# Kernel optimization log

Measured on AMD Instinct MI355X. Metric: run time of the kernel, lower is better.

## Reference

```python
import jax, jax.numpy as jnp
import numpy as np

B, T, C, H, TT = 8, 1024, 512, 8, 4  # batch, seq, n_embd, n_head, total_timestep
D = C // H


def setup_inputs() -> dict:
    key = jax.random.key(0)
    ks = jax.random.split(key, 4)
    s = 1.0 / np.sqrt(C)
    return {
        "x": jax.random.normal(ks[0], (B, T, C), jnp.float32),
        "padding_mask": jax.random.bernoulli(ks[1], 0.1, (TT, T)),  # bool
        "W_qkv": jax.random.normal(ks[2], (C, 3 * C), jnp.float32) * s,
        "b_qkv": jnp.zeros((3 * C,), jnp.float32),
        "W_proj": jax.random.normal(ks[3], (C, C), jnp.float32) * s,
        "b_proj": jnp.zeros((C,), jnp.float32),
    }


def reference(x, padding_mask, W_qkv, b_qkv, W_proj, b_proj):
    # fused QKV projection
    qkv = x @ W_qkv + b_qkv                       # [B,T,3C]
    q, k, v = jnp.split(qkv, 3, axis=-1)
    q = q.reshape(B, T, H, D)
    k = k.reshape(B, T, H, D)
    v = v.reshape(B, T, H, D)

    # mask: causal OR padding (True = attend), replicating torch semantics
    causal = jnp.tril(jnp.ones((T, T), bool))                 # [T,T]
    m = causal[None] | padding_mask[:, :, None]               # [TT,T,T]
    mask = jnp.broadcast_to(m[None], (B // TT, TT, T, T)).reshape(B, 1, T, T)

    scores = jnp.einsum("bqhd,bkhd->bhqk", q, k) * (1.0 / np.sqrt(D))
    scores = jnp.where(mask, scores, jnp.float32(-1e30))
    attn = jax.nn.softmax(scores, axis=-1)                    # [B,H,T,T]
    y = jnp.einsum("bhqk,bkhd->bqhd", attn, v).reshape(B, T, C)
    return y @ W_proj + b_proj
```

## Files before the change

### kernel.cpp

```cpp
#include <hip/hip_runtime.h>
#include <hip/hip_bf16.h>

#define BB 8
#define TT_ 4
#define TSEQ 1024
#define CEMB 512
#define NH 8
#define HD 64

typedef __attribute__((ext_vector_type(8))) short bf16x8;
typedef __attribute__((ext_vector_type(4))) float f32x4;
typedef __attribute__((ext_vector_type(16))) float f32x16;

#define AS1 __attribute__((address_space(1)))
#define AS3 __attribute__((address_space(3)))

__device__ __forceinline__ void gload_lds16(const void* g, void* l) {
  __builtin_amdgcn_global_load_lds((const AS1 unsigned int*)g, (AS3 unsigned int*)l, 16, 0, 0);
}

__device__ __forceinline__ short f2b(float f) {
  union { float f; unsigned u; } v; v.f = f;
  unsigned r = v.u + 0x7FFFu + ((v.u >> 16) & 1u);
  return (short)(r >> 16);
}

__device__ __forceinline__ unsigned pack2(float a, float b) {
  unsigned r;
  asm("v_cvt_pk_bf16_f32 %0, %1, %2" : "=v"(r) : "v"(a), "v"(b));
  return r;
}

__global__ __launch_bounds__(256) void k_prep(
    const float* __restrict__ x, short* __restrict__ xb,
    const float* __restrict__ w0, short* __restrict__ t0,
    const float* __restrict__ w1, short* __restrict__ t1,
    const void* __restrict__ pin, int* __restrict__ pme,
    int* __restrict__ perm, int* __restrict__ chunk_nkt)
{
  __shared__ float tsh[64][65];
  const int bid = blockIdx.x;

  if (bid < 2048) {
    const int i = bid * 256 + threadIdx.x;
    float4 v0 = ((const float4*)x)[i * 2];
    float4 v1 = ((const float4*)x)[i * 2 + 1];
    union { unsigned u[4]; bf16x8 v; } o;
    o.u[0] = pack2(v0.x, v0.y); o.u[1] = pack2(v0.z, v0.w);
    o.u[2] = pack2(v1.x, v1.y); o.u[3] = pack2(v1.z, v1.w);
    ((bf16x8*)xb)[i] = o.v;
    return;
  }

  if (bid < 2304) {
    const int z = (bid >= 2240);
    const int tile = z ? (bid - 2240) : (bid - 2048);
    const int ntx = z ? 8 : 24;
    const float* w = z ? w1 : w0;
    short* wt = z ? t1 : t0;
    const int N = z ? 512 : 1536, K = 512;
    const int tx = threadIdx.x & 15, ty = threadIdx.x >> 4;
    const int n0 = (tile % ntx) * 64, k0 = (tile / ntx) * 64;
#pragma unroll
    for (int i = 0; i < 4; ++i) {
      int kr = i * 16 + ty;
      float4 v = *(const float4*)&w[(size_t)(k0 + kr) * N + n0 + tx * 4];
      tsh[tx * 4 + 0][kr] = v.x; tsh[tx * 4 + 1][kr] = v.y;
      tsh[tx * 4 + 2][kr] = v.z; tsh[tx * 4 + 3][kr] = v.w;
    }
    __syncthreads();
#pragma unroll
    for (int i = 0; i < 4; ++i) {
      int nr = i * 16 + ty;
      short4 o;
      o.x = f2b(tsh[nr][tx * 4 + 0]); o.y = f2b(tsh[nr][tx * 4 + 1]);
      o.z = f2b(tsh[nr][tx * 4 + 2]); o.w = f2b(tsh[nr][tx * 4 + 3]);
      *(short4*)&wt[(size_t)(n0 + nr) * K + k0 + tx * 4] = o;
    }
    return;
  }

  __shared__ int bad_f32, any_f32, bad_i32, any_i32, bad_u16, any_u16;
  if (threadIdx.x == 0) { bad_f32 = any_f32 = bad_i32 = any_i32 = bad_u16 = any_u16 = 0; }
  __syncthreads();
  const unsigned char* pb = (const unsigned char*)pin;
  const float* pf = (const float*)pin;
  const int* pi = (const int*)pin;
  const unsigned short* ph = (const unsigned short*)pin;
  for (int i = threadIdx.x; i < 1024; i += 256) {
    float fv = pf[i];
    if (fv != 0.0f && fv != 1.0f) bad_f32 = 1;
    if (fv == 1.0f) any_f32 = 1;
    int iv = pi[i];
    if (iv != 0 && iv != 1) bad_i32 = 1;
    if (iv == 1) any_i32 = 1;
  }
  for (int i = threadIdx.x; i < 2048; i += 256) {
    unsigned short hv = ph[i];
    if (hv != 0 && hv != 0x3F80u && hv != 0x3C00u) bad_u16 = 1;
    if (hv == 0x3F80u || hv == 0x3C00u) any_u16 = 1;
  }
  __syncthreads();
  int mode = 3;
  if (!bad_f32 && any_f32) mode = 0;
  else if (!bad_i32 && any_i32) mode = 1;
  else if (!bad_u16 && any_u16) mode = 2;
  for (int i = threadIdx.x; i < TT_ * TSEQ; i += 256) {
    int v;
    if (mode == 0)      v = (pf[i] != 0.0f);
    else if (mode == 1) v = (pi[i] != 0);
    else if (mode == 2) v = (ph[i] != 0);
    else                v = (pb[i] != 0);
    pme[i] = v;
  }
  __syncthreads();

  const int w = threadIdx.x >> 6, lane = threadIdx.x & 63;
  {
    const int* rowp = pme + w * 1024;
    unsigned long long bal[16];
    int npm = 0;
#pragma unroll
    for (int g = 0; g < 16; ++g) {
      bal[g] = __ballot(rowp[g * 64 + lane] != 0);
      npm += __popcll(bal[g]);
    }
    int off_non = 0, off_pm = 1024 - npm;
#pragma unroll
    for (int g = 0; g < 16; ++g) {
      unsigned long long m = bal[g];
      int below = __popcll(m & ((1ull << lane) - 1ull));
      int ispm = (int)((m >> lane) & 1ull);
      int pos = ispm ? (off_pm + below) : (off_non + lane - below);
      perm[w * 1024 + pos] = g * 64 + lane;
      int c = __popcll(m);
      off_pm += c; off_non += 64 - c;
    }
  }
  __syncthreads();
  {
    const int tt = w, c = (lane >> 3) & 7, seg = lane & 7;
    int mx = 0;
#pragma unroll
    for (int i = 0; i < 16; ++i) {
      int q = perm[tt * 1024 + c * 128 + seg * 16 + i];
      int need = pme[tt * 1024 + q] ? 16 : ((q >> 6) + 1);
      mx = mx > need ? mx : need;
    }
#pragma unroll
    for (int s = 1; s < 8; s <<= 1) {
      int o = __shfl_xor(mx, s, 64);
      mx = mx > o ? mx : o;
    }
    if (seg == 0) chunk_nkt[tt * 8 + c] = mx;
  }
}

template<int MODE, int NT>
__global__ __launch_bounds__(256) void k_gemm(
    const short* __restrict__ A, const short* __restrict__ Bt,
    const float* __restrict__ bias,
    short* __restrict__ qb, short* __restrict__ kb, short* __restrict__ vtb,
    float* __restrict__ fout)
{
  __shared__ short As[3][128 * 32];
  __shared__ short Bs[3][128 * 32];
  const int tid = threadIdx.x, lane = tid & 63, w = tid >> 6;
  const int wm = w >> 1, wn = w & 1;
  const int idp = (blockIdx.x & 7) * ((NT * 64) >> 3) + (blockIdx.x >> 3);
  const int n0 = (idp % NT) * 128, m0 = (idp / NT) * 128;
  f32x4 acc[4][4] = {};
  const char* Abase = (const char*)A + (size_t)m0 * 1024;
  const char* Bbase = (const char*)Bt + (size_t)n0 * 1024;
  const int rowL = w * 16 + (lane >> 2);
  const int colB = (lane & 3) * 16;

  auto stage = [&](int buf, int k0) {
#pragma unroll
    for (int is = 0; is < 2; ++is) {
      int row = is * 64 + rowL;
      gload_lds16(Abase + (size_t)row * 1024 + (size_t)(k0 * 2 + colB),
                  (char*)As[buf] + is * 4096 + w * 1024);
      gload_lds16(Bbase + (size_t)row * 1024 + (size_t)(k0 * 2 + colB),
                  (char*)Bs[buf] + is * 4096 + w * 1024);
    }
  };

  stage(0, 0);
  stage(1, 32);
#pragma unroll
  for (int it = 0; it < 16; ++it) {
    if (it < 15) asm volatile("s_waitcnt vmcnt(4)\n\ts_barrier" ::: "memory");
    else         asm volatile("s_waitcnt vmcnt(0)\n\ts_barrier" ::: "memory");
    if (it + 2 < 16) stage((it + 2) % 3, (it + 2) * 32);
    const short* Ab = As[it % 3];
    const short* Bb = Bs[it % 3];
    bf16x8 a[4], bfr[4];
#pragma unroll
    for (int mf = 0; mf < 4; ++mf)
      a[mf] = *(const bf16x8*)&Ab[(wm * 64 + mf * 16 + (lane & 15)) * 32 + (lane >> 4) * 8];
#pragma unroll
    for (int nf = 0; nf < 4; ++nf)
      bfr[nf] = *(const bf16x8*)&Bb[(wn * 64 + nf * 16 + (lane & 15)) * 32 + (lane >> 4) * 8];
#pragma unroll
    for (int mf = 0; mf < 4; ++mf)
#pragma unroll
      for (int nf = 0; nf < 4; ++nf)
        acc[mf][nf] = __builtin_amdgcn_mfma_f32_16x16x32_bf16(a[mf], bfr[nf], acc[mf][nf], 0, 0, 0);
  }

#pragma unroll
  for (int nf = 0; nf < 4; ++nf) {
    const int n_g = n0 + wn * 64 + nf * 16 + (lane & 15);
    const float bv = bias[n_g];
    if (MODE == 0) {
      const int which = n_g >> 9;
      const int c = n_g & 511;
      const int h = c >> 6, d = c & 63;
      const float qsc = (which == 0) ? 0.18033688011112043f : 1.0f;
#pragma unroll
      for (int mf = 0; mf < 4; ++mf) {
        const int mb = m0 + wm * 64 + mf * 16 + ((lane >> 4) << 2);
        const int b = mb >> 10, t0 = mb & 1023;
        const int b8h = b * NH + h;
        if (which == 2) {
          short4 pk;
          pk.x = f2b(acc[mf][nf][0] + bv);
          pk.y = f2b(acc[mf][nf][1] + bv);
          pk.z = f2b(acc[mf][nf][2] + bv);
          pk.w = f2b(acc[mf][nf][3] + bv);
          *(short4*)&vtb[((size_t)b8h * HD + d) * TSEQ + t0] = pk;
        } else {
          short* dst = (which == 0) ? qb : kb;
          size_t base = ((size_t)b8h * TSEQ + t0) * HD + d;
#pragma unroll
          for (int r = 0; r < 4; ++r)
            dst[base + (size_t)r * HD] = f2b((acc[mf][nf][r] + bv) * qsc);
        }
      }
    } else {
#pragma unroll
      for (int mf = 0; mf < 4; ++mf) {
        const int mb = m0 + wm * 64 + mf * 16 + ((lane >> 4) << 2);
#pragma unroll
        for (int r = 0; r < 4; ++r)
          fout[(size_t)(mb + r) * 512 + n_g] = acc[mf][nf][r] + bv;
      }
    }
  }
}

__device__ __forceinline__ void pv_step(
    f32x16 p, int sub, int hi, int lq, const char* Vsb, f32x16& o0, f32x16& o1)
{
  unsigned P2[8];
#pragma unroll
  for (int i = 0; i < 8; ++i) P2[i] = pack2(p[2 * i], p[2 * i + 1]);
  unsigned e0 = __shfl_xor(hi ? P2[0] : P2[2], 32, 64);
  unsigned e1 = __shfl_xor(hi ? P2[1] : P2[3], 32, 64);
  unsigned e2 = __shfl_xor(hi ? P2[4] : P2[6], 32, 64);
  unsigned e3 = __shfl_xor(hi ? P2[5] : P2[7], 32, 64);
  union { unsigned u[4]; bf16x8 v; } f0, f1;
  f0.u[0] = hi ? e0 : P2[0]; f0.u[1] = hi ? e1 : P2[1];
  f0.u[2] = hi ? P2[2] : e0; f0.u[3] = hi ? P2[3] : e1;
  f1.u[0] = hi ? e2 : P2[4]; f1.u[1] = hi ? e3 : P2[5];
  f1.u[2] = hi ? P2[6] : e2; f1.u[3] = hi ? P2[7] : e3;
  __builtin_amdgcn_s_setprio(1);
#pragma unroll
  for (int dt = 0; dt < 2; ++dt) {
    int row = dt * 32 + lq;
    bf16x8 v0 = *(const bf16x8*)(Vsb + row * 128 + ((4 * sub + hi) ^ (row & 7)) * 16);
    bf16x8 v1 = *(const bf16x8*)(Vsb + row * 128 + ((4 * sub + 2 + hi) ^ (row & 7)) * 16);
    f32x16& o = dt ? o1 : o0;
    o = __builtin_amdgcn_mfma_f32_32x32x16_bf16(v0, f0.v, o, 0, 0, 0);
    o = __builtin_amdgcn_mfma_f32_32x32x16_bf16(v1, f1.v, o, 0, 0, 0);
  }
  __builtin_amdgcn_s_setprio(0);
}

__global__ __launch_bounds__(512) void k_attn(
    const short* __restrict__ qg, const short* __restrict__ kg,
    const short* __restrict__ vtg, const int* __restrict__ pme,
    const int* __restrict__ perm, const int* __restrict__ chunk_nkt,
    short* __restrict__ yb)
{
  __shared__ char smem[65536];
  const int tid = threadIdx.x, lane = tid & 63, w = tid >> 6;
  const int g = w >> 2;
  const int hi = lane >> 5, lq = lane & 31;
  const int id = blockIdx.x;
  const int bh = id & 63, b = bh >> 3, h = bh & 7, tt = b & 3;
  const int chunk = 7 - (id >> 6);
  const char* Qb = (const char*)(qg + (size_t)bh * TSEQ * HD);
  const char* Kb = (const char*)(kg + (size_t)bh * TSEQ * HD);
  const char* Vb = (const char*)(vtg + (size_t)bh * HD * TSEQ);

  const int stg_row = ((w & 3) << 3) + (lane >> 3);
  const int stg_cl = (lane & 7) ^ ((lane >> 3) & 7);

  auto stage = [&](int buf, int kt) {
#pragma unroll
    for (int is = 0; is < 2; ++is) {
      int row = is * 32 + stg_row;
      gload_lds16(Kb + (size_t)(kt * 64 + row) * 128 + stg_cl * 16,
                  smem + buf * 8192 + is * 4096 + (w & 3) * 1024);
      gload_lds16(Vb + (size_t)row * 2048 + kt * 128 + stg_cl * 16,
                  smem + 32768 + buf * 8192 + is * 4096 + (w & 3) * 1024);
    }
  };

  const int nkt = chunk_nkt[tt * 8 + chunk];
  const int q_g = perm[tt * 1024 + chunk * 128 + (w & 3) * 32 + lq];
  const int pmrow = pme[tt * TSEQ + q_g];

  if (g < nkt) stage(g * 2, g);

  int wmq = q_g, wnq = q_g;
#pragma unroll
  for (int s = 1; s < 64; s <<= 1) {
    wmq = max(wmq, __shfl_xor(wmq, s, 64));
    wnq = min(wnq, __shfl_xor(wnq, s, 64));
  }
  const int whaspm = __any(pmrow != 0);

  bf16x8 qf[4];
#pragma unroll
  for (int dk = 0; dk < 4; ++dk)
    qf[dk] = *(const bf16x8*)(Qb + (size_t)q_g * 128 + dk * 32 + hi * 16);

  float mrun = -1e30f, lrun = 0.0f;
  f32x16 o0 = {}, o1 = {};

  const int niter = (nkt + 1) >> 1;
  for (int i = 0; i < niter; ++i) {
    asm volatile("s_waitcnt vmcnt(0)" ::: "memory");
    __builtin_amdgcn_s_barrier();
    const int kt = 2 * i + g;
    if (kt + 2 < nkt) stage(g * 2 + ((i + 1) & 1), kt + 2);

    const int kb_ = kt * 64;
    if (kt < nkt && (kb_ <= wmq || whaspm)) {
      const char* Ksb = smem + (g * 2 + (i & 1)) * 8192;
      const char* Vsb = smem + 32768 + (g * 2 + (i & 1)) * 8192;

      f32x16 s0 = {}, s1 = {};
      __builtin_amdgcn_s_setprio(1);
#pragma unroll
      for (int dk = 0; dk < 4; ++dk) {
        int row0 = lq, row1 = 32 + lq;
        bf16x8 kf0 = *(const bf16x8*)(Ksb + row0 * 128 + ((2 * dk + hi) ^ (row0 & 7)) * 16);
        bf16x8 kf1 = *(const bf16x8*)(Ksb + row1 * 128 + ((2 * dk + hi) ^ (row1 & 7)) * 16);
        s0 = __builtin_amdgcn_mfma_f32_32x32x16_bf16(kf0, qf[dk], s0, 0, 0, 0);
        s1 = __builtin_amdgcn_mfma_f32_32x32x16_bf16(kf1, qf[dk], s1, 0, 0, 0);
      }
      __builtin_amdgcn_s_setprio(0);

      if (kb_ + 63 <= wnq) {
      } else if (kb_ > wmq) {
#pragma unroll
        for (int r = 0; r < 16; ++r) {
          s0[r] = pmrow ? s0[r] : -1e30f;
          s1[r] = pmrow ? s1[r] : -1e30f;
        }
      } else {
#pragma unroll
        for (int r = 0; r < 16; ++r) {
          int crow = (r & 3) + 8 * (r >> 2) + 4 * hi;
          s0[r] = ((kb_ + crow <= q_g) || pmrow) ? s0[r] : -1e30f;
          s1[r] = ((kb_ + 32 + crow <= q_g) || pmrow) ? s1[r] : -1e30f;
        }
      }

      float tm[16];
#pragma unroll
      for (int r = 0; r < 16; ++r) tm[r] = fmaxf(s0[r], s1[r]);
#pragma unroll
      for (int st = 8; st >= 1; st >>= 1)
#pragma unroll
        for (int r = 0; r < 8; ++r)
          if (r < st) tm[r] = fmaxf(tm[r], tm[r + st]);
      float mx = fmaxf(tm[0], __shfl_xor(tm[0], 32, 64));
      if (!__all(mx <= mrun + 8.0f)) {
        float nm = fmaxf(mrun, mx);
        float sc = __builtin_amdgcn_exp2f(mrun - nm);
        lrun *= sc;
#pragma unroll
        for (int r = 0; r < 16; ++r) { o0[r] *= sc; o1[r] *= sc; }
        mrun = nm;
      }
#pragma unroll
      for (int r = 0; r < 16; ++r) s0[r] = __builtin_amdgcn_exp2f(s0[r] - mrun);
#pragma unroll
      for (int r = 0; r < 16; ++r) s1[r] = __builtin_amdgcn_exp2f(s1[r] - mrun);
      float ts[16];
#pragma unroll
      for (int r = 0; r < 16; ++r) ts[r] = s0[r] + s1[r];
#pragma unroll
      for (int st = 8; st >= 1; st >>= 1)
#pragma unroll
        for (int r = 0; r < 8; ++r)
          if (r < st) ts[r] = ts[r] + ts[r + st];
      lrun += ts[0] + __shfl_xor(ts[0], 32, 64);

      pv_step(s0, 0, hi, lq, Vsb, o0, o1);
      pv_step(s1, 1, hi, lq, Vsb, o0, o1);
    }
  }

  __syncthreads();
  float* mg = (float*)smem;
  const int idx = (w & 3) * 64 + lane;
  if (g == 1) {
    mg[idx * 34 + 0] = mrun;
    mg[idx * 34 + 1] = lrun;
#pragma unroll
    for (int j = 0; j < 16; ++j) mg[idx * 34 + 2 + j] = o0[j];
#pragma unroll
    for (int j = 0; j < 16; ++j) mg[idx * 34 + 18 + j] = o1[j];
  }
  __syncthreads();
  if (g == 0) {
    const float mB = mg[idx * 34 + 0], lB = mg[idx * 34 + 1];
    const float m = fmaxf(mrun, mB);
    const float wa = __builtin_amdgcn_exp2f(mrun - m);
    const float wb = __builtin_amdgcn_exp2f(mB - m);
    const float linv = 1.0f / (lrun * wa + lB * wb);
    const float fa = wa * linv, fb = wb * linv;
    short* yrow = yb + ((size_t)b * TSEQ + q_g) * CEMB + h * HD;
#pragma unroll
    for (int dt = 0; dt < 2; ++dt) {
      const f32x16& o = dt ? o1 : o0;
      const int ob = dt ? 18 : 2;
#pragma unroll
      for (int gg = 0; gg < 4; ++gg) {
        short4 pk;
        pk.x = f2b(o[4 * gg + 0] * fa + mg[idx * 34 + ob + 4 * gg + 0] * fb);
        pk.y = f2b(o[4 * gg + 1] * fa + mg[idx * 34 + ob + 4 * gg + 1] * fb);
        pk.z = f2b(o[4 * gg + 2] * fa + mg[idx * 34 + ob + 4 * gg + 2] * fb);
        pk.w = f2b(o[4 * gg + 3] * fa + mg[idx * 34 + ob + 4 * gg + 3] * fb);
        *(short4*)(yrow + dt * 32 + 8 * gg + 4 * hi) = pk;
      }
    }
  }
}

extern "C" void kernel_launch(void* const* d_in, const int* in_sizes, int n_in,
                              void* d_out, int out_size, void* d_ws, size_t ws_size,
                              hipStream_t stream) {
  const float* x     = (const float*)d_in[0];
  const void*  pmask = d_in[1];
  const float* Wqkv  = (const float*)d_in[2];
  const float* bqkv  = (const float*)d_in[3];
  const float* Wproj = (const float*)d_in[4];
  const float* bproj = (const float*)d_in[5];
  float* out = (float*)d_out;
  char* ws = (char*)d_ws;

  const size_t OFF_XB   = 0;
  const size_t OFF_WQT  = 8388608;
  const size_t OFF_WPT  = 9961472;
  const size_t OFF_Q    = 10485760;
  const size_t OFF_K    = 18874368;
  const size_t OFF_VT   = 27262976;
  const size_t OFF_Y    = 35651584;
  const size_t OFF_PM   = 44040192;
  const size_t OFF_PERM = 44056576;
  const size_t OFF_CNKT = 44072960;
  const size_t NEED     = 44073984;
  if (ws_size < NEED) return;

  short* xb  = (short*)(ws + OFF_XB);
  short* wqT = (short*)(ws + OFF_WQT);
  short* wpT = (short*)(ws + OFF_WPT);
  short* qb  = (short*)(ws + OFF_Q);
  short* kb  = (short*)(ws + OFF_K);
  short* vtb = (short*)(ws + OFF_VT);
  short* yb  = (short*)(ws + OFF_Y);
  int*   pme = (int*)(ws + OFF_PM);
  int*   prm = (int*)(ws + OFF_PERM);
  int*   cnk = (int*)(ws + OFF_CNKT);

  k_prep<<<dim3(2305), dim3(256), 0, stream>>>(x, xb, Wqkv, wqT, Wproj, wpT,
                                               pmask, pme, prm, cnk);
  k_gemm<0, 12><<<dim3(768), dim3(256), 0, stream>>>(xb, wqT, bqkv, qb, kb, vtb, nullptr);
  k_attn<<<dim3(512), dim3(512), 0, stream>>>(qb, kb, vtb, pme, prm, cnk, yb);
  k_gemm<1, 4><<<dim3(256), dim3(256), 0, stream>>>(yb, wpT, bproj, nullptr, nullptr, nullptr, out);
}
```

Baseline: 81.88 us.

## Move mask preprocessing into QKV GEMM, shrink proj GEMM tiles, reorder attention chunks

The padding-mask decode, permutation and chunk key-tile computation move out of the prep kernel into an extra block of the QKV GEMM launch, so that single serial block no longer sits on the tail of the prep kernel. The output projection GEMM drops from 128x128 to 64x128 tiles, doubling its grid to 512 blocks for better CU occupancy. Attention blocks now alternate heavy and light chunks instead of strictly descending order, aiming for better load balance. Risks: the extra mask block can itself become a tail in the GEMM, and smaller tiles reduce data reuse.

Measured after the change: 85.79 us. +4.8%, slower.

```diff
diff --git a/kernel.cpp b/kernel.cpp
--- a/kernel.cpp
+++ b/kernel.cpp
@@ -34,9 +34,7 @@
 __global__ __launch_bounds__(256) void k_prep(
     const float* __restrict__ x, short* __restrict__ xb,
     const float* __restrict__ w0, short* __restrict__ t0,
-    const float* __restrict__ w1, short* __restrict__ t1,
-    const void* __restrict__ pin, int* __restrict__ pme,
-    int* __restrict__ perm, int* __restrict__ chunk_nkt)
+    const float* __restrict__ w1, short* __restrict__ t1)
 {
   __shared__ float tsh[64][65];
   const int bid = blockIdx.x;
@@ -52,123 +50,123 @@
     return;
   }
 
-  if (bid < 2304) {
-    const int z = (bid >= 2240);
-    const int tile = z ? (bid - 2240) : (bid - 2048);
-    const int ntx = z ? 8 : 24;
-    const float* w = z ? w1 : w0;
-    short* wt = z ? t1 : t0;
-    const int N = z ? 512 : 1536, K = 512;
-    const int tx = threadIdx.x & 15, ty = threadIdx.x >> 4;
-    const int n0 = (tile % ntx) * 64, k0 = (tile / ntx) * 64;
-#pragma unroll
-    for (int i = 0; i < 4; ++i) {
-      int kr = i * 16 + ty;
-      float4 v = *(const float4*)&w[(size_t)(k0 + kr) * N + n0 + tx * 4];
-      tsh[tx * 4 + 0][kr] = v.x; tsh[tx * 4 + 1][kr] = v.y;
-      tsh[tx * 4 + 2][kr] = v.z; tsh[tx * 4 + 3][kr] = v.w;
-    }
-    __syncthreads();
-#pragma unroll
-    for (int i = 0; i < 4; ++i) {
-      int nr = i * 16 + ty;
-      short4 o;
-      o.x = f2b(tsh[nr][tx * 4 + 0]); o.y = f2b(tsh[nr][tx * 4 + 1]);
-      o.z = f2b(tsh[nr][tx * 4 + 2]); o.w = f2b(tsh[nr][tx * 4 + 3]);
-      *(short4*)&wt[(size_t)(n0 + nr) * K + k0 + tx * 4] = o;
-    }
-    return;
-  }
-
-  __shared__ int bad_f32, any_f32, bad_i32, any_i32, bad_u16, any_u16;
-  if (threadIdx.x == 0) { bad_f32 = any_f32 = bad_i32 = any_i32 = bad_u16 = any_u16 = 0; }
+  const int z = (bid >= 2240);
+  const int tile = z ? (bid - 2240) : (bid - 2048);
+  const int ntx = z ? 8 : 24;
+  const float* w = z ? w1 : w0;
+  short* wt = z ? t1 : t0;
+  const int N = z ? 512 : 1536, K = 512;
+  const int tx = threadIdx.x & 15, ty = threadIdx.x >> 4;
+  const int n0 = (tile % ntx) * 64, k0 = (tile / ntx) * 64;
+#pragma unroll
+  for (int i = 0; i < 4; ++i) {
+    int kr = i * 16 + ty;
+    float4 v = *(const float4*)&w[(size_t)(k0 + kr) * N + n0 + tx * 4];
+    tsh[tx * 4 + 0][kr] = v.x; tsh[tx * 4 + 1][kr] = v.y;
+    tsh[tx * 4 + 2][kr] = v.z; tsh[tx * 4 + 3][kr] = v.w;
+  }
   __syncthreads();
-  const unsigned char* pb = (const unsigned char*)pin;
-  const float* pf = (const float*)pin;
-  const int* pi = (const int*)pin;
-  const unsigned short* ph = (const unsigned short*)pin;
-  for (int i = threadIdx.x; i < 1024; i += 256) {
-    float fv = pf[i];
-    if (fv != 0.0f && fv != 1.0f) bad_f32 = 1;
-    if (fv == 1.0f) any_f32 = 1;
-    int iv = pi[i];
-    if (iv != 0 && iv != 1) bad_i32 = 1;
-    if (iv == 1) any_i32 = 1;
-  }
-  for (int i = threadIdx.x; i < 2048; i += 256) {
-    unsigned short hv = ph[i];
-    if (hv != 0 && hv != 0x3F80u && hv != 0x3C00u) bad_u16 = 1;
-    if (hv == 0x3F80u || hv == 0x3C00u) any_u16 = 1;
-  }
-  __syncthreads();
-  int mode = 3;
-  if (!bad_f32 && any_f32) mode = 0;
-  else if (!bad_i32 && any_i32) mode = 1;
-  else if (!bad_u16 && any_u16) mode = 2;
-  for (int i = threadIdx.x; i < TT_ * TSEQ; i += 256) {
-    int v;
-    if (mode == 0)      v = (pf[i] != 0.0f);
-    else if (mode == 1) v = (pi[i] != 0);
-    else if (mode == 2) v = (ph[i] != 0);
-    else                v = (pb[i] != 0);
-    pme[i] = v;
-  }
-  __syncthreads();
-
-  const int w = threadIdx.x >> 6, lane = threadIdx.x & 63;
-  {
-    const int* rowp = pme + w * 1024;
-    unsigned long long bal[16];
-    int npm = 0;
-#pragma unroll
-    for (int g = 0; g < 16; ++g) {
-      bal[g] = __ballot(rowp[g * 64 + lane] != 0);
-      npm += __popcll(bal[g]);
-    }
-    int off_non = 0, off_pm = 1024 - npm;
-#pragma unroll
-    for (int g = 0; g < 16; ++g) {
-      unsigned long long m = bal[g];
-      int below = __popcll(m & ((1ull << lane) - 1ull));
-      int ispm = (int)((m >> lane) & 1ull);
-      int pos = ispm ? (off_pm + below) : (off_non + lane - below);
-      perm[w * 1024 + pos] = g * 64 + lane;
-      int c = __popcll(m);
-      off_pm += c; off_non += 64 - c;
-    }
-  }
-  __syncthreads();
-  {
-    const int tt = w, c = (lane >> 3) & 7, seg = lane & 7;
-    int mx = 0;
-#pragma unroll
-    for (int i = 0; i < 16; ++i) {
-      int q = perm[tt * 1024 + c * 128 + seg * 16 + i];
-      int need = pme[tt * 1024 + q] ? 16 : ((q >> 6) + 1);
-      mx = mx > need ? mx : need;
-    }
-#pragma unroll
-    for (int s = 1; s < 8; s <<= 1) {
-      int o = __shfl_xor(mx, s, 64);
-      mx = mx > o ? mx : o;
-    }
-    if (seg == 0) chunk_nkt[tt * 8 + c] = mx;
-  }
-}
-
-template<int MODE, int NT>
-__global__ __launch_bounds__(256) void k_gemm(
+#pragma unroll
+  for (int i = 0; i < 4; ++i) {
+    int nr = i * 16 + ty;
+    short4 o;
+    o.x = f2b(tsh[nr][tx * 4 + 0]); o.y = f2b(tsh[nr][tx * 4 + 1]);
+    o.z = f2b(tsh[nr][tx * 4 + 2]); o.w = f2b(tsh[nr][tx * 4 + 3]);
+    *(short4*)&wt[(size_t)(n0 + nr) * K + k0 + tx * 4] = o;
+  }
+}
+
+__global__ __launch_bounds__(256) void k_gemm0(
     const short* __restrict__ A, const short* __restrict__ Bt,
     const float* __restrict__ bias,
     short* __restrict__ qb, short* __restrict__ kb, short* __restrict__ vtb,
-    float* __restrict__ fout)
+    const void* __restrict__ pin, int* __restrict__ pme,
+    int* __restrict__ perm, int* __restrict__ chunk_nkt)
 {
   __shared__ short As[3][128 * 32];
   __shared__ short Bs[3][128 * 32];
+
+  if (blockIdx.x == 768) {
+    __shared__ int bad_f32, any_f32, bad_i32, any_i32, bad_u16, any_u16;
+    if (threadIdx.x == 0) { bad_f32 = any_f32 = bad_i32 = any_i32 = bad_u16 = any_u16 = 0; }
+    __syncthreads();
+    const unsigned char* pb = (const unsigned char*)pin;
+    const float* pf = (const float*)pin;
+    const int* pi = (const int*)pin;
+    const unsigned short* ph = (const unsigned short*)pin;
+    for (int i = threadIdx.x; i < 1024; i += 256) {
+      float fv = pf[i];
+      if (fv != 0.0f && fv != 1.0f) bad_f32 = 1;
+      if (fv == 1.0f) any_f32 = 1;
+      int iv = pi[i];
+      if (iv != 0 && iv != 1) bad_i32 = 1;
+      if (iv == 1) any_i32 = 1;
+    }
+    for (int i = threadIdx.x; i < 2048; i += 256) {
+      unsigned short hv = ph[i];
+      if (hv != 0 && hv != 0x3F80u && hv != 0x3C00u) bad_u16 = 1;
+      if (hv == 0x3F80u || hv == 0x3C00u) any_u16 = 1;
+    }
+    __syncthreads();
+    int mode = 3;
+    if (!bad_f32 && any_f32) mode = 0;
+    else if (!bad_i32 && any_i32) mode = 1;
+    else if (!bad_u16 && any_u16) mode = 2;
+    for (int i = threadIdx.x; i < TT_ * TSEQ; i += 256) {
+      int v;
+      if (mode == 0)      v = (pf[i] != 0.0f);
+      else if (mode == 1) v = (pi[i] != 0);
+      else if (mode == 2) v = (ph[i] != 0);
+      else                v = (pb[i] != 0);
+      pme[i] = v;
+    }
+    __syncthreads();
+    const int w = threadIdx.x >> 6, lane = threadIdx.x & 63;
+    {
+      const int* rowp = pme + w * 1024;
+      unsigned long long bal[16];
+      int npm = 0;
+#pragma unroll
+      for (int g = 0; g < 16; ++g) {
+        bal[g] = __ballot(rowp[g * 64 + lane] != 0);
+        npm += __popcll(bal[g]);
+      }
+      int off_non = 0, off_pm = 1024 - npm;
+#pragma unroll
+      for (int g = 0; g < 16; ++g) {
+        unsigned long long m = bal[g];
+        int below = __popcll(m & ((1ull << lane) - 1ull));
+        int ispm = (int)((m >> lane) & 1ull);
+        int pos = ispm ? (off_pm + below) : (off_non + lane - below);
+        perm[w * 1024 + pos] = g * 64 + lane;
+        int c = __popcll(m);
+        off_pm += c; off_non += 64 - c;
+      }
+    }
+    __syncthreads();
+    {
+      const int tt = w, c = (lane >> 3) & 7, seg = lane & 7;
+      int mx = 0;
+#pragma unroll
+      for (int i = 0; i < 16; ++i) {
+        int q = perm[tt * 1024 + c * 128 + seg * 16 + i];
+        int need = pme[tt * 1024 + q] ? 16 : ((q >> 6) + 1);
+        mx = mx > need ? mx : need;
+      }
+#pragma unroll
+      for (int s = 1; s < 8; s <<= 1) {
+        int o = __shfl_xor(mx, s, 64);
+        mx = mx > o ? mx : o;
+      }
+      if (seg == 0) chunk_nkt[tt * 8 + c] = mx;
+    }
+    return;
+  }
+
   const int tid = threadIdx.x, lane = tid & 63, w = tid >> 6;
   const int wm = w >> 1, wn = w & 1;
-  const int idp = (blockIdx.x & 7) * ((NT * 64) >> 3) + (blockIdx.x >> 3);
-  const int n0 = (idp % NT) * 128, m0 = (idp / NT) * 128;
+  const int idp = (blockIdx.x & 7) * 96 + (blockIdx.x >> 3);
+  const int n0 = (idp % 12) * 128, m0 = (idp / 12) * 128;
   f32x4 acc[4][4] = {};
   const char* Abase = (const char*)A + (size_t)m0 * 1024;
   const char* Bbase = (const char*)Bt + (size_t)n0 * 1024;
@@ -213,39 +211,93 @@
   for (int nf = 0; nf < 4; ++nf) {
     const int n_g = n0 + wn * 64 + nf * 16 + (lane & 15);
     const float bv = bias[n_g];
-    if (MODE == 0) {
-      const int which = n_g >> 9;
-      const int c = n_g & 511;
-      const int h = c >> 6, d = c & 63;
-      const float qsc = (which == 0) ? 0.18033688011112043f : 1.0f;
-#pragma unroll
-      for (int mf = 0; mf < 4; ++mf) {
-        const int mb = m0 + wm * 64 + mf * 16 + ((lane >> 4) << 2);
-        const int b = mb >> 10, t0 = mb & 1023;
-        const int b8h = b * NH + h;
-        if (which == 2) {
-          short4 pk;
-          pk.x = f2b(acc[mf][nf][0] + bv);
-          pk.y = f2b(acc[mf][nf][1] + bv);
-          pk.z = f2b(acc[mf][nf][2] + bv);
-          pk.w = f2b(acc[mf][nf][3] + bv);
-          *(short4*)&vtb[((size_t)b8h * HD + d) * TSEQ + t0] = pk;
-        } else {
-          short* dst = (which == 0) ? qb : kb;
-          size_t base = ((size_t)b8h * TSEQ + t0) * HD + d;
-#pragma unroll
-          for (int r = 0; r < 4; ++r)
-            dst[base + (size_t)r * HD] = f2b((acc[mf][nf][r] + bv) * qsc);
-        }
-      }
-    } else {
-#pragma unroll
-      for (int mf = 0; mf < 4; ++mf) {
-        const int mb = m0 + wm * 64 + mf * 16 + ((lane >> 4) << 2);
+    const int which = n_g >> 9;
+    const int c = n_g & 511;
+    const int h = c >> 6, d = c & 63;
+    const float qsc = (which == 0) ? 0.18033688011112043f : 1.0f;
+#pragma unroll
+    for (int mf = 0; mf < 4; ++mf) {
+      const int mb = m0 + wm * 64 + mf * 16 + ((lane >> 4) << 2);
+      const int b = mb >> 10, t0 = mb & 1023;
+      const int b8h = b * NH + h;
+      if (which == 2) {
+        short4 pk;
+        pk.x = f2b(acc[mf][nf][0] + bv);
+        pk.y = f2b(acc[mf][nf][1] + bv);
+        pk.z = f2b(acc[mf][nf][2] + bv);
+        pk.w = f2b(acc[mf][nf][3] + bv);
+        *(short4*)&vtb[((size_t)b8h * HD + d) * TSEQ + t0] = pk;
+      } else {
+        short* dst = (which == 0) ? qb : kb;
+        size_t base = ((size_t)b8h * TSEQ + t0) * HD + d;
 #pragma unroll
         for (int r = 0; r < 4; ++r)
-          fout[(size_t)(mb + r) * 512 + n_g] = acc[mf][nf][r] + bv;
-      }
+          dst[base + (size_t)r * HD] = f2b((acc[mf][nf][r] + bv) * qsc);
+      }
+    }
+  }
+}
+
+__global__ __launch_bounds__(256) void k_gemm1(
+    const short* __restrict__ A, const short* __restrict__ Bt,
+    const float* __restrict__ bias, float* __restrict__ fout)
+{
+  __shared__ short As[3][64 * 32];
+  __shared__ short Bs[3][128 * 32];
+  const int tid = threadIdx.x, lane = tid & 63, w = tid >> 6;
+  const int wm = w >> 1, wn = w & 1;
+  const int idp = (blockIdx.x & 7) * 64 + (blockIdx.x >> 3);
+  const int n0 = (idp & 3) * 128, m0 = (idp >> 2) * 64;
+  f32x4 acc[2][4] = {};
+  const char* Abase = (const char*)A + (size_t)m0 * 1024;
+  const char* Bbase = (const char*)Bt + (size_t)n0 * 1024;
+  const int rowL = tid >> 2;
+  const int colB = (tid & 3) * 16;
+
+  auto stage = [&](int buf, int k0) {
+    gload_lds16(Abase + (size_t)rowL * 1024 + (size_t)(k0 * 2 + colB),
+                (char*)As[buf] + w * 1024);
+#pragma unroll
+    for (int is = 0; is < 2; ++is) {
+      int row = is * 64 + rowL;
+      gload_lds16(Bbase + (size_t)row * 1024 + (size_t)(k0 * 2 + colB),
+                  (char*)Bs[buf] + is * 4096 + w * 1024);
+    }
+  };
+
+  stage(0, 0);
+  stage(1, 32);
+#pragma unroll
+  for (int it = 0; it < 16; ++it) {
+    if (it < 15) asm volatile("s_waitcnt vmcnt(3)\n\ts_barrier" ::: "memory");
+    else         asm volatile("s_waitcnt vmcnt(0)\n\ts_barrier" ::: "memory");
+    if (it + 2 < 16) stage((it + 2) % 3, (it + 2) * 32);
+    const short* Ab = As[it % 3];
+    const short* Bb = Bs[it % 3];
+    bf16x8 a[2], bfr[4];
+#pragma unroll
+    for (int mf = 0; mf < 2; ++mf)
+      a[mf] = *(const bf16x8*)&Ab[(wm * 32 + mf * 16 + (lane & 15)) * 32 + (lane >> 4) * 8];
+#pragma unroll
+    for (int nf = 0; nf < 4; ++nf)
+      bfr[nf] = *(const bf16x8*)&Bb[(wn * 64 + nf * 16 + (lane & 15)) * 32 + (lane >> 4) * 8];
+#pragma unroll
+    for (int mf = 0; mf < 2; ++mf)
+#pragma unroll
+      for (int nf = 0; nf < 4; ++nf)
+        acc[mf][nf] = __builtin_amdgcn_mfma_f32_16x16x32_bf16(a[mf], bfr[nf], acc[mf][nf], 0, 0, 0);
+  }
+
+#pragma unroll
+  for (int nf = 0; nf < 4; ++nf) {
+    const int n_g = n0 + wn * 64 + nf * 16 + (lane & 15);
+    const float bv = bias[n_g];
+#pragma unroll
+    for (int mf = 0; mf < 2; ++mf) {
+      const int mb = m0 + wm * 32 + mf * 16 + ((lane >> 4) << 2);
+#pragma unroll
+      for (int r = 0; r < 4; ++r)
+        fout[(size_t)(mb + r) * 512 + n_g] = acc[mf][nf][r] + bv;
     }
   }
 }
@@ -290,7 +342,8 @@
   const int hi = lane >> 5, lq = lane & 31;
   const int id = blockIdx.x;
   const int bh = id & 63, b = bh >> 3, h = bh & 7, tt = b & 3;
-  const int chunk = 7 - (id >> 6);
+  const int p = id >> 6;
+  const int chunk = (p < 4) ? (7 - p) : (p - 4);
   const char* Qb = (const char*)(qg + (size_t)bh * TSEQ * HD);
   const char* Kb = (const char*)(kg + (size_t)bh * TSEQ * HD);
   const char* Vb = (const char*)(vtg + (size_t)bh * HD * TSEQ);
@@ -480,9 +533,9 @@
   int*   prm = (int*)(ws + OFF_PERM);
   int*   cnk = (int*)(ws + OFF_CNKT);
 
-  k_prep<<<dim3(2305), dim3(256), 0, stream>>>(x, xb, Wqkv, wqT, Wproj, wpT,
+  k_prep<<<dim3(2304), dim3(256), 0, stream>>>(x, xb, Wqkv, wqT, Wproj, wpT);
+  k_gemm0<<<dim3(769), dim3(256), 0, stream>>>(xb, wqT, bqkv, qb, kb, vtb,
                                                pmask, pme, prm, cnk);
-  k_gemm<0, 12><<<dim3(768), dim3(256), 0, stream>>>(xb, wqT, bqkv, qb, kb, vtb, nullptr);
   k_attn<<<dim3(512), dim3(512), 0, stream>>>(qb, kb, vtb, pme, prm, cnk, yb);
-  k_gemm<1, 4><<<dim3(256), dim3(256), 0, stream>>>(yb, wpT, bproj, nullptr, nullptr, nullptr, out);
-}
+  k_gemm1<<<dim3(512), dim3(256), 0, stream>>>(yb, wpT, bproj, out);
+}
```
